# Kernel optimization log

Hardware: AMD Instinct MI355X
Metric: run time of the kernel (lower is better)

The kernel has to match this reference:

```python
import jax, jax.numpy as jnp
import numpy as np
import math

BATCH, CLS, ATT_DIM, IMG_DIM = 256, 500, 1024, 1024
ATT_HC, HIDDEN_C = 256, 1024
T_TEMP = 10.0
DEGREE = 30
THRESH = math.cos(math.pi * DEGREE / 180.0)
NEG = -9.0e15


def setup_inputs() -> dict:
    key = jax.random.key(0)
    ks = jax.random.split(key, 9)
    inp = {
        "image_feats": jax.random.normal(ks[0], (BATCH, IMG_DIM), dtype=jnp.float32),
        "attributes": jax.random.normal(ks[1], (CLS, ATT_DIM), dtype=jnp.float32),
        "unused": 0,
        # learned parameters (kaiming-like scaling)
        "att_g": jax.random.normal(ks[2], (ATT_DIM, ATT_HC), dtype=jnp.float32) / math.sqrt(ATT_DIM),
        "img_w": jax.random.normal(ks[3], (IMG_DIM, HIDDEN_C), dtype=jnp.float32) / math.sqrt(IMG_DIM),
        "sem_w": jax.random.normal(ks[4], (ATT_DIM, HIDDEN_C), dtype=jnp.float32) / math.sqrt(ATT_DIM),
        "sem_b": jax.random.normal(ks[5], (1, HIDDEN_C), dtype=jnp.float32) / math.sqrt(IMG_DIM),
        "fc_w": jax.random.normal(ks[6], (1, HIDDEN_C), dtype=jnp.float32) / math.sqrt(HIDDEN_C),
        "fc_b": jax.random.normal(ks[7], (1,), dtype=jnp.float32) / math.sqrt(HIDDEN_C),
    }
    return inp


def _get_new_attribute(attributes, att_g):
    # project attributes, cosine similarity between all class pairs
    g = attributes @ att_g                                    # [cls, att_hC]
    gn = g / jnp.linalg.norm(g, axis=1, keepdims=True)        # row-normalize
    sim = gn @ gn.T                                           # [cls, cls] cosine sims
    raw = jnp.where(sim > THRESH, sim, NEG)                   # angular-threshold mask
    attention = jax.nn.softmax(raw * T_TEMP, axis=1)          # [cls, cls]
    return attention @ attributes                             # [cls, att_dim]


def reference(image_feats, attributes, unused, att_g, img_w, sem_w, sem_b, fc_w, fc_b):
    att_outs = _get_new_attribute(attributes, att_g)          # [cls, att_dim]
    # factor the broadcast: identical math to matmul on expanded tensors
    img_h = image_feats @ img_w                               # [batch, hidden]
    sem_h = att_outs @ sem_w                                  # [cls, hidden]
    hidden = jax.nn.relu(img_h[:, None, :] + sem_h[None, :, :] + sem_b[None, :, :])  # [batch, cls, hidden]
    out = jnp.einsum('bch,h->bc', hidden, fc_w[0]) + fc_b[0]  # [batch, cls]
    return out
```

## Files before the change

kernel.cpp:

```cpp
#include <hip/hip_runtime.h>
#include <math.h>

#define BATCH 256
#define CLS 500
#define HIDDEN_ 1024
#define T_TEMP_ 10.0f
#define THRESH_ 0.86602540378443864676f
#define NEGV -9.0e15f

typedef __attribute__((ext_vector_type(8))) short short8;
typedef __attribute__((ext_vector_type(8))) unsigned short u16x8;
typedef __attribute__((ext_vector_type(4))) float f32x4;

static __device__ __forceinline__ unsigned short f2bf(float x) {
    unsigned int u = __builtin_bit_cast(unsigned int, x);
    u += 0x7fff + ((u >> 16) & 1);
    return (unsigned short)(u >> 16);
}
static __device__ __forceinline__ u16x8 pack8(const float4& a, const float4& b) {
    u16x8 o;
    o[0] = f2bf(a.x); o[1] = f2bf(a.y); o[2] = f2bf(a.z); o[3] = f2bf(a.w);
    o[4] = f2bf(b.x); o[5] = f2bf(b.y); o[6] = f2bf(b.z); o[7] = f2bf(b.w);
    return o;
}

__global__ __launch_bounds__(256) void convert_kernel(
    const float* __restrict__ attrs, const float* __restrict__ imgf,
    const float* __restrict__ attg, const float* __restrict__ imgw,
    const float* __restrict__ semw,
    unsigned short* __restrict__ attrs_bf, unsigned short* __restrict__ imgf_bf,
    unsigned short* __restrict__ attgT, unsigned short* __restrict__ imgwT,
    unsigned short* __restrict__ semwT)
{
    __shared__ unsigned short tb[64][72];
    const int t = threadIdx.x;
    int bid = blockIdx.x;

    if (bid < 378) {
        const float* s; unsigned short* d; int idx;
        if (bid < 250) { s = attrs; d = attrs_bf; idx = bid * 2048 + t * 8; }
        else           { s = imgf;  d = imgf_bf;  idx = (bid - 250) * 2048 + t * 8; }
        float4 v0 = *(const float4*)&s[idx];
        float4 v1 = *(const float4*)&s[idx + 4];
        *(u16x8*)&d[idx] = pack8(v0, v1);
        return;
    }
    bid -= 378;
    const float* s; unsigned short* d; int Csz;
    if (bid < 64)       { s = attg; d = attgT; Csz = 256; }
    else if (bid < 320) { bid -= 64;  s = imgw; d = imgwT; Csz = 1024; }
    else                { bid -= 320; s = semw; d = semwT; Csz = 1024; }
    const int tiles_c = Csz >> 6;
    const int tr = bid / tiles_c, tc = bid % tiles_c;
    {
        const int r = t >> 2, cq = (t & 3) * 16;
        const float* p = &s[(size_t)(tr * 64 + r) * Csz + tc * 64 + cq];
        float4 v0 = *(const float4*)(p);
        float4 v1 = *(const float4*)(p + 4);
        float4 v2 = *(const float4*)(p + 8);
        float4 v3 = *(const float4*)(p + 12);
        *(u16x8*)&tb[r][cq]     = pack8(v0, v1);
        *(u16x8*)&tb[r][cq + 8] = pack8(v2, v3);
    }
    __syncthreads();
    {
        const int c = t >> 2, r0 = (t & 3) * 16;
        u16x8 o0, o1;
        #pragma unroll
        for (int i = 0; i < 8; ++i) { o0[i] = tb[r0 + i][c]; o1[i] = tb[r0 + 8 + i][c]; }
        unsigned short* q = &d[(size_t)(tc * 64 + c) * 1024 + tr * 64 + r0];
        *(u16x8*)q = o0;
        *(u16x8*)(q + 8) = o1;
    }
}

__global__ __launch_bounds__(256) void mfma_gemm_bf(
    const unsigned short* __restrict__ A1, int alim1,
    const unsigned short* __restrict__ A2, int a2t0, int alim2,
    const unsigned short* __restrict__ B1, const unsigned short* __restrict__ B2,
    float* __restrict__ C, int M, int N, int K, int klen)
{
    __shared__ unsigned short As[64][40];
    __shared__ unsigned short Bs[128][40];

    const int t  = threadIdx.x;
    const int bx = blockIdx.x;
    const int n0 = blockIdx.y * 128;
    const int k0 = blockIdx.z * klen;

    const unsigned short* A; const unsigned short* B; int ar0, alim;
    if (bx < a2t0) { A = A1; B = B1; ar0 = bx * 64;          alim = alim1; }
    else           { A = A2; B = B2; ar0 = (bx - a2t0) * 64; alim = alim2; }

    const int w = t >> 6, lane = t & 63;
    const int wr = w >> 1, wc = w & 1;
    const int fr = lane & 15, kg = lane >> 4;

    const int a_row = t >> 2, a_k = (t & 3) * 8;
    const int b_row = t >> 1, b_k = (t & 1) * 16;
    const int gra = ar0 + a_row;
    const int grb = n0 + b_row;
    const bool va = gra < alim;
    const bool vb = grb < N;
    const size_t abase = (size_t)gra * K + a_k;
    const size_t bbase = (size_t)grb * K + b_k;

    u16x8 zz = {0,0,0,0,0,0,0,0};
    u16x8 pa = zz, pb0 = zz, pb1 = zz;
    if (va) pa = *(const u16x8*)&A[abase + k0];
    if (vb) { pb0 = *(const u16x8*)&B[bbase + k0]; pb1 = *(const u16x8*)&B[bbase + k0 + 8]; }

    f32x4 zero4 = {0.f, 0.f, 0.f, 0.f};
    f32x4 acc[2][4];
    #pragma unroll
    for (int i = 0; i < 2; ++i)
        #pragma unroll
        for (int j = 0; j < 4; ++j) acc[i][j] = zero4;

    for (int kb = k0; kb < k0 + klen; kb += 32) {
        *(u16x8*)&As[a_row][a_k] = pa;
        *(u16x8*)&Bs[b_row][b_k] = pb0;
        *(u16x8*)&Bs[b_row][b_k + 8] = pb1;
        __syncthreads();

        const int kn = kb + 32;
        if (kn < k0 + klen) {
            if (va) pa = *(const u16x8*)&A[abase + kn];
            if (vb) { pb0 = *(const u16x8*)&B[bbase + kn]; pb1 = *(const u16x8*)&B[bbase + kn + 8]; }
        }

        short8 af[2], bfr[4];
        #pragma unroll
        for (int i = 0; i < 2; ++i)
            af[i] = *(short8*)&As[wr * 32 + i * 16 + fr][kg * 8];
        #pragma unroll
        for (int j = 0; j < 4; ++j)
            bfr[j] = *(short8*)&Bs[wc * 64 + j * 16 + fr][kg * 8];
        #pragma unroll
        for (int i = 0; i < 2; ++i)
            #pragma unroll
            for (int j = 0; j < 4; ++j)
                acc[i][j] = __builtin_amdgcn_mfma_f32_16x16x32_bf16(
                    af[i], bfr[j], acc[i][j], 0, 0, 0);
        __syncthreads();
    }

    float* Cw = C + (gridDim.z > 1 ? (size_t)blockIdx.z * M * N : 0);
    const int orow0 = bx * 64 + wr * 32, ocol0 = n0 + wc * 64;
    #pragma unroll
    for (int i = 0; i < 2; ++i) {
        const int r0 = orow0 + i * 16 + kg * 4;
        #pragma unroll
        for (int j = 0; j < 4; ++j) {
            const int cc = ocol0 + j * 16 + fr;
            if (cc >= N) continue;
            #pragma unroll
            for (int r = 0; r < 4; ++r) {
                const int rr = r0 + r;
                if (rr < M) Cw[(size_t)rr * N + cc] = acc[i][j][r];
            }
        }
    }
}

__global__ __launch_bounds__(256) void reduce_norm_kernel(
    const float* __restrict__ part, unsigned short* __restrict__ gn_bf)
{
    const int c = blockIdx.x, t = threadIdx.x;
    float v = 0.f;
    #pragma unroll
    for (int z = 0; z < 8; ++z) v += part[(size_t)z * (CLS * 256) + c * 256 + t];
    float ss = v * v;
    #pragma unroll
    for (int off = 32; off >= 1; off >>= 1) ss += __shfl_down(ss, off);
    __shared__ float red[4];
    const int wave = t >> 6, lane = t & 63;
    if (lane == 0) red[wave] = ss;
    __syncthreads();
    const float tot = red[0] + red[1] + red[2] + red[3];
    const float rn  = 1.f / sqrtf(tot);
    gn_bf[c * 256 + t] = f2bf(v * rn);
}

__global__ __launch_bounds__(256) void softmax_att_kernel(
    const float* __restrict__ sim, const float* __restrict__ attrs,
    unsigned short* __restrict__ att_outs)
{
    const int c = blockIdx.x, t = threadIdx.x;
    __shared__ float p_s[512];
    __shared__ float redm[4];
    __shared__ float reds[4];

    const float d0 = sim[(size_t)c * CLS + t];
    const float d1 = (t + 256 < CLS) ? sim[(size_t)c * CLS + t + 256] : NEGV;

    float vmax = fmaxf((d0 > THRESH_) ? d0 : NEGV, (d1 > THRESH_) ? d1 : NEGV);
    #pragma unroll
    for (int off = 32; off >= 1; off >>= 1) vmax = fmaxf(vmax, __shfl_down(vmax, off));
    const int wave = t >> 6, lane = t & 63;
    if (lane == 0) redm[wave] = vmax;
    __syncthreads();
    const float m = fmaxf(fmaxf(redm[0], redm[1]), fmaxf(redm[2], redm[3]));

    const float p0 = (d0 > THRESH_) ? expf(T_TEMP_ * (d0 - m)) : 0.f;
    const float p1 = (d1 > THRESH_) ? expf(T_TEMP_ * (d1 - m)) : 0.f;
    p_s[t] = p0;
    p_s[t + 256] = p1;
    float vsum = p0 + p1;
    #pragma unroll
    for (int off = 32; off >= 1; off >>= 1) vsum += __shfl_down(vsum, off);
    if (lane == 0) reds[wave] = vsum;
    __syncthreads();
    const float inv = 1.f / (reds[0] + reds[1] + reds[2] + reds[3]);

    float acc[4] = {0.f, 0.f, 0.f, 0.f};
    for (int base = 0; base < 512; base += 64) {
        const float pv_l = p_s[base + lane];
        unsigned long long mask = __ballot(pv_l > 0.f);
        while (mask) {
            const int l = __ffsll((long long)mask) - 1;
            mask &= mask - 1;
            const int c2 = base + l;
            const float pv = p_s[c2];
            const float* ar = &attrs[(size_t)c2 * 1024 + t];
            #pragma unroll
            for (int j = 0; j < 4; ++j) acc[j] += pv * ar[256 * j];
        }
    }
    #pragma unroll
    for (int j = 0; j < 4; ++j)
        att_outs[(size_t)c * 1024 + t + 256 * j] = f2bf(acc[j] * inv);
}

__global__ __launch_bounds__(256) void fused_out_partial(
    const float* __restrict__ part, int ks, const float* __restrict__ sem_b,
    const float* __restrict__ fc_w, float* __restrict__ outpart, int h_per)
{
    __shared__ float imgs[64][68];
    __shared__ float sems[64][68];
    __shared__ float fcs[128];

    const size_t pstride = (size_t)756 * 1024;
    const int t  = threadIdx.x;
    const int tb = t >> 4, tc = t & 15;
    const int b0 = blockIdx.x * 64, c0 = blockIdx.y * 64;
    const int h0 = blockIdx.z * h_per;

    if (t < (h_per >> 2)) *(float4*)&fcs[t * 4] = *(const float4*)&fc_w[h0 + t * 4];

    float acc[4][4] = {};

    for (int hs = 0; hs < (h_per >> 6); ++hs) {
        const int hb = h0 + hs * 64;
        #pragma unroll
        for (int i = 0; i < 4; ++i) {
            const int row = (t >> 4) + 16 * i;
            const int col = (t & 15) * 4;
            float4 iv = make_float4(0.f, 0.f, 0.f, 0.f);
            const float* pi = &part[(size_t)(b0 + row) * 1024 + hb + col];
            for (int z = 0; z < ks; ++z) {
                float4 vz = *(const float4*)(pi + z * pstride);
                iv.x += vz.x; iv.y += vz.y; iv.z += vz.z; iv.w += vz.w;
            }
            *(float4*)&imgs[row][col] = iv;

            float4 sv = make_float4(0.f, 0.f, 0.f, 0.f);
            if (c0 + row < CLS) {
                const float* ps = &part[(size_t)(256 + c0 + row) * 1024 + hb + col];
                for (int z = 0; z < ks; ++z) {
                    float4 vz = *(const float4*)(ps + z * pstride);
                    sv.x += vz.x; sv.y += vz.y; sv.z += vz.z; sv.w += vz.w;
                }
                float4 bb = *(const float4*)&sem_b[hb + col];
                sv.x += bb.x; sv.y += bb.y; sv.z += bb.z; sv.w += bb.w;
            }
            *(float4*)&sems[row][col] = sv;
        }
        __syncthreads();

        #pragma unroll
        for (int h4 = 0; h4 < 16; ++h4) {
            float4 ia[4], sa[4];
            #pragma unroll
            for (int i = 0; i < 4; ++i) ia[i] = *(float4*)&imgs[tb + 16 * i][h4 * 4];
            #pragma unroll
            for (int j = 0; j < 4; ++j) sa[j] = *(float4*)&sems[tc + 16 * j][h4 * 4];
            #pragma unroll
            for (int e = 0; e < 4; ++e) {
                const float w2 = fcs[hs * 64 + h4 * 4 + e];
                #pragma unroll
                for (int i = 0; i < 4; ++i) {
                    const float iv = (&ia[i].x)[e];
                    #pragma unroll
                    for (int j = 0; j < 4; ++j) {
                        const float sv = (&sa[j].x)[e];
                        acc[i][j] += fmaxf(iv + sv, 0.f) * w2;
                    }
                }
            }
        }
        __syncthreads();
    }

    const int nh = blockIdx.z;
    #pragma unroll
    for (int i = 0; i < 4; ++i) {
        const int b = b0 + tb + 16 * i;
        #pragma unroll
        for (int j = 0; j < 4; ++j) {
            const int cc = c0 + tc + 16 * j;
            if (cc < CLS)
                outpart[((size_t)nh * BATCH + b) * CLS + cc] = acc[i][j];
        }
    }
}

__global__ __launch_bounds__(256) void finalize_kernel(
    const float* __restrict__ partial, const float* __restrict__ fc_b,
    float* __restrict__ out, int nsplit)
{
    const int idx = blockIdx.x * 256 + threadIdx.x;
    if (idx >= BATCH * CLS) return;
    float s = fc_b[0];
    for (int nh = 0; nh < nsplit; ++nh)
        s += partial[(size_t)nh * BATCH * CLS + idx];
    out[idx] = s;
}

extern "C" void kernel_launch(void* const* d_in, const int* in_sizes, int n_in,
                              void* d_out, int out_size, void* d_ws, size_t ws_size,
                              hipStream_t stream)
{
    const float* image_feats = (const float*)d_in[0];
    const float* attributes  = (const float*)d_in[1];
    const float* att_g       = (const float*)d_in[3];
    const float* img_w       = (const float*)d_in[4];
    const float* sem_w       = (const float*)d_in[5];
    const float* sem_b       = (const float*)d_in[6];
    const float* fc_w        = (const float*)d_in[7];
    const float* fc_b        = (const float*)d_in[8];
    float* out = (float*)d_out;

    char* ws = (char*)d_ws;
    size_t off = 0;
    auto alloc = [&](size_t b) { size_t o = off; off = (off + b + 255) & ~(size_t)255; return o; };
    const size_t o_attr = alloc((size_t)500 * 1024 * 2);
    const size_t o_imgf = alloc((size_t)256 * 1024 * 2);
    const size_t o_attg = alloc((size_t)256 * 1024 * 2);
    const size_t o_imgw = alloc((size_t)1024 * 1024 * 2);
    const size_t o_semw = alloc((size_t)1024 * 1024 * 2);
    const size_t o_gn   = alloc((size_t)500 * 256 * 2);
    const size_t o_atto = alloc((size_t)500 * 1024 * 2);
    const size_t o_gp   = alloc((size_t)8 * 500 * 256 * 4);
    const size_t base   = off;

    int ks = 4, nh = 16;
    while (base + (size_t)ks * 756 * 1024 * 4 + (size_t)nh * BATCH * CLS * 4 + 512 > ws_size) {
        if (ks > 1) ks >>= 1;
        else if (nh > 8) nh = 8;
        else break;
    }
    const size_t o_hidp = alloc((size_t)ks * 756 * 1024 * 4);
    const size_t o_outp = alloc((size_t)nh * BATCH * CLS * 4);
    (void)o_outp;

    unsigned short* attr_bf = (unsigned short*)(ws + o_attr);
    unsigned short* imgf_bf = (unsigned short*)(ws + o_imgf);
    unsigned short* attgT   = (unsigned short*)(ws + o_attg);
    unsigned short* imgwT   = (unsigned short*)(ws + o_imgw);
    unsigned short* semwT   = (unsigned short*)(ws + o_semw);
    unsigned short* gn_bf   = (unsigned short*)(ws + o_gn);
    unsigned short* atto_bf = (unsigned short*)(ws + o_atto);
    float* gpart_sim        = (float*)(ws + o_gp);
    float* hidP             = (float*)(ws + o_hidp);
    float* outP             = (float*)(ws + o_outp);

    convert_kernel<<<954, 256, 0, stream>>>(
        attributes, image_feats, att_g, img_w, sem_w,
        attr_bf, imgf_bf, attgT, imgwT, semwT);

    mfma_gemm_bf<<<dim3(8, 2, 8), 256, 0, stream>>>(
        attr_bf, 500, attr_bf, 1000, 500, attgT, attgT,
        gpart_sim, CLS, 256, 1024, 128);

    reduce_norm_kernel<<<CLS, 256, 0, stream>>>(gpart_sim, gn_bf);

    mfma_gemm_bf<<<dim3(8, 4, 1), 256, 0, stream>>>(
        gn_bf, 500, gn_bf, 1000, 500, gn_bf, gn_bf,
        gpart_sim, CLS, CLS, 256, 256);

    softmax_att_kernel<<<CLS, 256, 0, stream>>>(gpart_sim, attributes, atto_bf);

    mfma_gemm_bf<<<dim3(12, 8, ks), 256, 0, stream>>>(
        imgf_bf, 256, atto_bf, 4, 500, imgwT, semwT,
        hidP, 756, 1024, 1024, 1024 / ks);

    fused_out_partial<<<dim3(BATCH / 64, (CLS + 63) / 64, nh), 256, 0, stream>>>(
        hidP, ks, sem_b, fc_w, outP, HIDDEN_ / nh);

    finalize_kernel<<<(BATCH * CLS + 255) / 256, 256, 0, stream>>>(outP, fc_b, out, nh);
}
```

Measured before the change: 68.11 us.

## Store split-K hidden partials as bf16 and pack fused-output math into float2

The split-K GEMM that produces image and semantic hidden partials now writes bf16 instead of fp32, which halves the workspace traffic that the fused output kernel reads back. The fused kernel converts bf16 to float when summing the partials. Its inner relu-weighted accumulation now uses 2-wide float vectors, which can map to packed FP32 instructions, and it loads the fc weights as a float4. Rounding each split-K partial to bf16 adds error to the hidden activations before the relu.

```diff
diff --git a/kernel.cpp b/kernel.cpp
--- a/kernel.cpp
+++ b/kernel.cpp
@@ -10,12 +10,17 @@
 
 typedef __attribute__((ext_vector_type(8))) short short8;
 typedef __attribute__((ext_vector_type(8))) unsigned short u16x8;
+typedef __attribute__((ext_vector_type(4))) unsigned short u16x4;
 typedef __attribute__((ext_vector_type(4))) float f32x4;
+typedef __attribute__((ext_vector_type(2))) float f32x2;
 
 static __device__ __forceinline__ unsigned short f2bf(float x) {
     unsigned int u = __builtin_bit_cast(unsigned int, x);
     u += 0x7fff + ((u >> 16) & 1);
     return (unsigned short)(u >> 16);
+}
+static __device__ __forceinline__ float bf2f(unsigned short v) {
+    return __builtin_bit_cast(float, (unsigned int)v << 16);
 }
 static __device__ __forceinline__ u16x8 pack8(const float4& a, const float4& b) {
     u16x8 o;
@@ -78,7 +83,8 @@
     const unsigned short* __restrict__ A1, int alim1,
     const unsigned short* __restrict__ A2, int a2t0, int alim2,
     const unsigned short* __restrict__ B1, const unsigned short* __restrict__ B2,
-    float* __restrict__ C, int M, int N, int K, int klen)
+    float* __restrict__ C, unsigned short* __restrict__ Cbf,
+    int M, int N, int K, int klen)
 {
     __shared__ unsigned short As[64][40];
     __shared__ unsigned short Bs[128][40];
@@ -145,19 +151,37 @@
         __syncthreads();
     }
 
-    float* Cw = C + (gridDim.z > 1 ? (size_t)blockIdx.z * M * N : 0);
     const int orow0 = bx * 64 + wr * 32, ocol0 = n0 + wc * 64;
-    #pragma unroll
-    for (int i = 0; i < 2; ++i) {
-        const int r0 = orow0 + i * 16 + kg * 4;
-        #pragma unroll
-        for (int j = 0; j < 4; ++j) {
-            const int cc = ocol0 + j * 16 + fr;
-            if (cc >= N) continue;
-            #pragma unroll
-            for (int r = 0; r < 4; ++r) {
-                const int rr = r0 + r;
-                if (rr < M) Cw[(size_t)rr * N + cc] = acc[i][j][r];
+    if (Cbf) {
+        unsigned short* Cw = Cbf + (size_t)blockIdx.z * M * N;
+        #pragma unroll
+        for (int i = 0; i < 2; ++i) {
+            const int r0 = orow0 + i * 16 + kg * 4;
+            #pragma unroll
+            for (int j = 0; j < 4; ++j) {
+                const int cc = ocol0 + j * 16 + fr;
+                if (cc >= N) continue;
+                #pragma unroll
+                for (int r = 0; r < 4; ++r) {
+                    const int rr = r0 + r;
+                    if (rr < M) Cw[(size_t)rr * N + cc] = f2bf(acc[i][j][r]);
+                }
+            }
+        }
+    } else {
+        float* Cw = C + (gridDim.z > 1 ? (size_t)blockIdx.z * M * N : 0);
+        #pragma unroll
+        for (int i = 0; i < 2; ++i) {
+            const int r0 = orow0 + i * 16 + kg * 4;
+            #pragma unroll
+            for (int j = 0; j < 4; ++j) {
+                const int cc = ocol0 + j * 16 + fr;
+                if (cc >= N) continue;
+                #pragma unroll
+                for (int r = 0; r < 4; ++r) {
+                    const int rr = r0 + r;
+                    if (rr < M) Cw[(size_t)rr * N + cc] = acc[i][j][r];
+                }
             }
         }
     }
@@ -233,7 +257,7 @@
 }
 
 __global__ __launch_bounds__(256) void fused_out_partial(
-    const float* __restrict__ part, int ks, const float* __restrict__ sem_b,
+    const unsigned short* __restrict__ part, int ks, const float* __restrict__ sem_b,
     const float* __restrict__ fc_w, float* __restrict__ outpart, int h_per)
 {
     __shared__ float imgs[64][68];
@@ -248,7 +272,11 @@
 
     if (t < (h_per >> 2)) *(float4*)&fcs[t * 4] = *(const float4*)&fc_w[h0 + t * 4];
 
-    float acc[4][4] = {};
+    f32x2 acc2[4][4];
+    #pragma unroll
+    for (int i = 0; i < 4; ++i)
+        #pragma unroll
+        for (int j = 0; j < 4; ++j) acc2[i][j] = (f32x2){0.f, 0.f};
 
     for (int hs = 0; hs < (h_per >> 6); ++hs) {
         const int hb = h0 + hs * 64;
@@ -256,25 +284,27 @@
         for (int i = 0; i < 4; ++i) {
             const int row = (t >> 4) + 16 * i;
             const int col = (t & 15) * 4;
-            float4 iv = make_float4(0.f, 0.f, 0.f, 0.f);
-            const float* pi = &part[(size_t)(b0 + row) * 1024 + hb + col];
+            f32x4 iv = {0.f, 0.f, 0.f, 0.f};
+            const unsigned short* pi = &part[(size_t)(b0 + row) * 1024 + hb + col];
             for (int z = 0; z < ks; ++z) {
-                float4 vz = *(const float4*)(pi + z * pstride);
-                iv.x += vz.x; iv.y += vz.y; iv.z += vz.z; iv.w += vz.w;
+                u16x4 vz = *(const u16x4*)(pi + (size_t)z * pstride);
+                iv[0] += bf2f(vz[0]); iv[1] += bf2f(vz[1]);
+                iv[2] += bf2f(vz[2]); iv[3] += bf2f(vz[3]);
             }
-            *(float4*)&imgs[row][col] = iv;
-
-            float4 sv = make_float4(0.f, 0.f, 0.f, 0.f);
+            *(f32x4*)&imgs[row][col] = iv;
+
+            f32x4 sv = {0.f, 0.f, 0.f, 0.f};
             if (c0 + row < CLS) {
-                const float* ps = &part[(size_t)(256 + c0 + row) * 1024 + hb + col];
+                const unsigned short* ps = &part[(size_t)(256 + c0 + row) * 1024 + hb + col];
                 for (int z = 0; z < ks; ++z) {
-                    float4 vz = *(const float4*)(ps + z * pstride);
-                    sv.x += vz.x; sv.y += vz.y; sv.z += vz.z; sv.w += vz.w;
+                    u16x4 vz = *(const u16x4*)(ps + (size_t)z * pstride);
+                    sv[0] += bf2f(vz[0]); sv[1] += bf2f(vz[1]);
+                    sv[2] += bf2f(vz[2]); sv[3] += bf2f(vz[3]);
                 }
                 float4 bb = *(const float4*)&sem_b[hb + col];
-                sv.x += bb.x; sv.y += bb.y; sv.z += bb.z; sv.w += bb.w;
+                sv[0] += bb.x; sv[1] += bb.y; sv[2] += bb.z; sv[3] += bb.w;
             }
-            *(float4*)&sems[row][col] = sv;
+            *(f32x4*)&sems[row][col] = sv;
         }
         __syncthreads();
 
@@ -285,18 +315,25 @@
             for (int i = 0; i < 4; ++i) ia[i] = *(float4*)&imgs[tb + 16 * i][h4 * 4];
             #pragma unroll
             for (int j = 0; j < 4; ++j) sa[j] = *(float4*)&sems[tc + 16 * j][h4 * 4];
-            #pragma unroll
-            for (int e = 0; e < 4; ++e) {
-                const float w2 = fcs[hs * 64 + h4 * 4 + e];
+            const float4 wv = *(const float4*)&fcs[hs * 64 + h4 * 4];
+            #pragma unroll
+            for (int e2 = 0; e2 < 2; ++e2) {
+                const f32x2 w2 = {(&wv.x)[2 * e2], (&wv.x)[2 * e2 + 1]};
+                f32x2 ia2[4], sa2[4];
                 #pragma unroll
-                for (int i = 0; i < 4; ++i) {
-                    const float iv = (&ia[i].x)[e];
+                for (int i = 0; i < 4; ++i)
+                    ia2[i] = (f32x2){(&ia[i].x)[2 * e2], (&ia[i].x)[2 * e2 + 1]};
+                #pragma unroll
+                for (int j = 0; j < 4; ++j)
+                    sa2[j] = (f32x2){(&sa[j].x)[2 * e2], (&sa[j].x)[2 * e2 + 1]};
+                #pragma unroll
+                for (int i = 0; i < 4; ++i)
                     #pragma unroll
                     for (int j = 0; j < 4; ++j) {
-                        const float sv = (&sa[j].x)[e];
-                        acc[i][j] += fmaxf(iv + sv, 0.f) * w2;
+                        f32x2 s = ia2[i] + sa2[j];
+                        s = __builtin_elementwise_max(s, (f32x2){0.f, 0.f});
+                        acc2[i][j] += s * w2;
                     }
-                }
             }
         }
         __syncthreads();
@@ -310,7 +347,7 @@
         for (int j = 0; j < 4; ++j) {
             const int cc = c0 + tc + 16 * j;
             if (cc < CLS)
-                outpart[((size_t)nh * BATCH + b) * CLS + cc] = acc[i][j];
+                outpart[((size_t)nh * BATCH + b) * CLS + cc] = acc2[i][j][0] + acc2[i][j][1];
         }
     }
 }
@@ -355,12 +392,12 @@
     const size_t base   = off;
 
     int ks = 4, nh = 16;
-    while (base + (size_t)ks * 756 * 1024 * 4 + (size_t)nh * BATCH * CLS * 4 + 512 > ws_size) {
+    while (base + (size_t)ks * 756 * 1024 * 2 + (size_t)nh * BATCH * CLS * 4 + 512 > ws_size) {
         if (ks > 1) ks >>= 1;
         else if (nh > 8) nh = 8;
         else break;
     }
-    const size_t o_hidp = alloc((size_t)ks * 756 * 1024 * 4);
+    const size_t o_hidp = alloc((size_t)ks * 756 * 1024 * 2);
     const size_t o_outp = alloc((size_t)nh * BATCH * CLS * 4);
     (void)o_outp;
 
@@ -372,7 +409,7 @@
     unsigned short* gn_bf   = (unsigned short*)(ws + o_gn);
     unsigned short* atto_bf = (unsigned short*)(ws + o_atto);
     float* gpart_sim        = (float*)(ws + o_gp);
-    float* hidP             = (float*)(ws + o_hidp);
+    unsigned short* hidP    = (unsigned short*)(ws + o_hidp);
     float* outP             = (float*)(ws + o_outp);
 
     convert_kernel<<<954, 256, 0, stream>>>(
@@ -381,19 +418,19 @@
 
     mfma_gemm_bf<<<dim3(8, 2, 8), 256, 0, stream>>>(
         attr_bf, 500, attr_bf, 1000, 500, attgT, attgT,
-        gpart_sim, CLS, 256, 1024, 128);
+        gpart_sim, nullptr, CLS, 256, 1024, 128);
 
     reduce_norm_kernel<<<CLS, 256, 0, stream>>>(gpart_sim, gn_bf);
 
     mfma_gemm_bf<<<dim3(8, 4, 1), 256, 0, stream>>>(
         gn_bf, 500, gn_bf, 1000, 500, gn_bf, gn_bf,
-        gpart_sim, CLS, CLS, 256, 256);
+        gpart_sim, nullptr, CLS, CLS, 256, 256);
 
     softmax_att_kernel<<<CLS, 256, 0, stream>>>(gpart_sim, attributes, atto_bf);
 
     mfma_gemm_bf<<<dim3(12, 8, ks), 256, 0, stream>>>(
         imgf_bf, 256, atto_bf, 4, 500, imgwT, semwT,
-        hidP, 756, 1024, 1024, 1024 / ks);
+        nullptr, hidP, 756, 1024, 1024, 1024 / ks);
 
     fused_out_partial<<<dim3(BATCH / 64, (CLS + 63) / 64, nh), 256, 0, stream>>>(
         hidP, ks, sem_b, fc_w, outP, HIDDEN_ / nh);
```

New measurement: 66.07 us. 1.03x faster.
